# Kernel optimization log

Measured on AMD Instinct MI355X. Metric: run time of the kernel, lower is better.

Reference implementation:

```python
import jax, jax.numpy as jnp
import numpy as np

B, K, D = 8, 4000, 256
H, DQ, DV = 8, 32, 32
WIN, PAD = 200, 50
STEP = WIN - 2 * PAD  # 100
BETA = 0.25


def setup_inputs() -> dict:
    key = jax.random.key(0)
    ks = jax.random.split(key, 14)
    s = 0.02
    return {
        "query": jax.random.normal(ks[0], (B, K, D), jnp.float32),
        "key": jax.random.normal(ks[1], (B, K, D), jnp.float32),
        "value": jax.random.normal(ks[2], (B, K, D), jnp.float32),
        "Wq": jax.random.normal(ks[3], (D, H * DQ), jnp.float32) * s,
        "bq": jax.random.normal(ks[4], (H * DQ,), jnp.float32) * s,
        "Wk": jax.random.normal(ks[5], (D, H * DQ), jnp.float32) * s,
        "bk": jax.random.normal(ks[6], (H * DQ,), jnp.float32) * s,
        "Wv": jax.random.normal(ks[7], (D, H * DV), jnp.float32) * s,
        "bv": jax.random.normal(ks[8], (H * DV,), jnp.float32) * s,
        "Wo": jax.random.normal(ks[9], (H * DV, D), jnp.float32) * s,
        "bo": jax.random.normal(ks[10], (D,), jnp.float32) * s,
    }


def _windows(x, n_win):
    starts = jnp.arange(n_win) * STEP
    idx = starts[:, None] + jnp.arange(WIN)[None, :]
    return x[:, :, idx, :]


def reference(query, key, value, Wq, bq, Wk, bk, Wv, bv, Wo, bo):
    b, k_len, d = query.shape
    pad = lambda t: jnp.pad(t, ((0, 0), (PAD, PAD), (0, 0)), mode='edge')  # replicate pad
    qp, kp, vp = pad(query), pad(key), pad(value)
    kpad = k_len + 2 * PAD
    n_win = (kpad - WIN) // STEP + 1

    def proj(x, Wm, bias, dh):
        y = x @ Wm + bias                       # [B, Kp, H*dh]
        return y.reshape(b, kpad, H, dh).transpose(0, 2, 1, 3)  # [B, H, Kp, dh]

    q = _windows(proj(qp, Wq, bq, DQ), n_win)
    kk = _windows(proj(kp, Wk, bk, DQ), n_win)
    v = _windows(proj(vp, Wv, bv, DV), n_win)

    scores = jnp.einsum('bhnid,bhnjd->bhnij', q, kk) / jnp.sqrt(jnp.float32(WIN))
    dist = jnp.abs(jnp.arange(WIN)[:, None] - jnp.arange(WIN)[None, :]).astype(scores.dtype)
    cauchy = (1.0 / (1.0 + BETA * dist * dist)) * (1.0 - jnp.eye(WIN, dtype=scores.dtype))
    scores = scores * cauchy
    causal = jnp.triu(jnp.ones((WIN, WIN), dtype=bool), k=1)  # attention_size is not None -> causal masking
    scores = jnp.where(causal, -jnp.inf, scores)
    attn = jax.nn.softmax(scores, axis=-1)
    out = jnp.einsum('bhnij,bhnjd->bhnid', attn, v)
    out = out[:, :, :, PAD:WIN - PAD, :].reshape(b, H, k_len, DV)
    out = out.transpose(0, 2, 1, 3).reshape(b, k_len, H * DV)  # heads concatenated, head-major slices
    return out @ Wo + bo
```

## Files before the change

kernel.cpp:

```cpp
#include <hip/hip_runtime.h>


typedef __bf16 bf16_t;
typedef __bf16 bf16x4 __attribute__((ext_vector_type(4)));
typedef __bf16 bf16x8 __attribute__((ext_vector_type(8)));
typedef float  f32x4  __attribute__((ext_vector_type(4)));

#define MFMA16(a, b, c) __builtin_amdgcn_mfma_f32_16x16x32_bf16((a), (b), (c), 0, 0, 0)

typedef __attribute__((address_space(1))) const unsigned char gas_u8;
typedef __attribute__((address_space(3))) unsigned char las_u8;

static __device__ __forceinline__ void gload16(const void* g, void* l) {
  __builtin_amdgcn_global_load_lds((gas_u8*)g, (las_u8*)l, 16, 0, 0);
}

static __device__ __forceinline__ bf16x4 cvt4(float4 a) {
  bf16x4 r;
  r[0] = (bf16_t)a.x; r[1] = (bf16_t)a.y; r[2] = (bf16_t)a.z; r[3] = (bf16_t)a.w;
  return r;
}

static __device__ __forceinline__ unsigned short bbits(bf16_t v) {
  union { bf16_t b; unsigned short u; } c; c.b = v; return c.u;
}

#define APITCH 264
#define ABYTES (64 * APITCH * 2)

__global__ __launch_bounds__(256)
void prep_weights(const float* __restrict__ Wq, const float* __restrict__ Wk,
                  const float* __restrict__ Wv, const float* __restrict__ Wo,
                  bf16_t* __restrict__ wt) {
  const int mat  = blockIdx.x >> 6;
  const int tile = blockIdx.x & 63;
  const int kt = (tile >> 3) * 32, nt = (tile & 7) * 32;
  const float* W = (mat == 0) ? Wq : (mat == 1) ? Wk : (mat == 2) ? Wv : Wo;
  __shared__ float t[32][33];
  const int tx = threadIdx.x & 31, ty = threadIdx.x >> 5;
#pragma unroll
  for (int i = 0; i < 32; i += 8)
    t[ty + i][tx] = W[(size_t)(kt + ty + i) * 256 + nt + tx];
  __syncthreads();
  bf16_t* dst = wt + (size_t)mat * 65536;
#pragma unroll
  for (int i = 0; i < 32; i += 8)
    dst[(size_t)(nt + ty + i) * 256 + kt + tx] = (bf16_t)t[tx][ty + i];
}

__global__ __launch_bounds__(256)
void proj_gemm(const float* __restrict__ qx, const float* __restrict__ kx,
               const float* __restrict__ vx, const bf16_t* __restrict__ wt,
               const float* __restrict__ bq, const float* __restrict__ bk,
               const float* __restrict__ bv,
               bf16_t* __restrict__ qb, bf16_t* __restrict__ kb,
               bf16_t* __restrict__ vt, int M, float qscale) {
  const int mode = blockIdx.y;
  const float* X    = (mode == 0) ? qx : (mode == 1) ? kx : vx;
  const float* bias = (mode == 0) ? bq : (mode == 1) ? bk : bv;
  const bf16_t* W   = wt + (size_t)mode * 65536;

  __shared__ __align__(16) char lds[ABYTES + 2 * 16384];
  bf16_t* laA = (bf16_t*)lds;
  char*   ldsB = lds + ABYTES;

  const int tid  = threadIdx.x;
  const int lane = tid & 63;
  const int w    = tid >> 6;
  const int lo   = lane & 15, hi = lane >> 4;
  const int m0   = blockIdx.x * 64;

  {
    const int colq = (tid & 63) * 4;
    const int r0   = tid >> 6;
#pragma unroll
    for (int u = 0; u < 16; ++u) {
      const int r = r0 + u * 4;
      int ar = m0 + r; if (ar >= M) ar = M - 1;
      const float4 v = *(const float4*)(X + (size_t)ar * 256 + colq);
      *(bf16x4*)&laA[r * APITCH + colq] = cvt4(v);
    }
  }

  const bf16_t* bsrc[4];
  int boff[4];
#pragma unroll
  for (int j = 0; j < 4; ++j) {
    const int s = (w * 4 + j) * 64 + lane;
    bsrc[j] = W + (size_t)(s >> 2) * 256 + ((s & 3) << 3);
    boff[j] = (w * 4 + j) * 1024;
  }
  int bbase[4];
#pragma unroll
  for (int ni = 0; ni < 4; ++ni)
    bbase[ni] = (w * 64 + ni * 16 + lo) * 64 + hi * 16;

#pragma unroll
  for (int j = 0; j < 4; ++j) gload16(bsrc[j], ldsB + boff[j]);
  __syncthreads();

  f32x4 acc[4][4] = {};

  for (int t = 0; t < 8; ++t) {
    const int cur = (t & 1) * 16384;
    if (t < 7) {
      const int nxt = ((t + 1) & 1) * 16384;
#pragma unroll
      for (int j = 0; j < 4; ++j) gload16(bsrc[j] + (t + 1) * 32, ldsB + nxt + boff[j]);
      asm volatile("s_waitcnt vmcnt(4)" ::: "memory");
    } else {
      asm volatile("s_waitcnt vmcnt(0)" ::: "memory");
    }
    __builtin_amdgcn_sched_barrier(0);
    __builtin_amdgcn_s_barrier();

    bf16x8 af[4], bfv[4];
#pragma unroll
    for (int mi = 0; mi < 4; ++mi)
      af[mi] = *(const bf16x8*)&laA[(mi * 16 + lo) * APITCH + t * 32 + hi * 8];
#pragma unroll
    for (int ni = 0; ni < 4; ++ni)
      bfv[ni] = *(const bf16x8*)(ldsB + cur + bbase[ni]);
#pragma unroll
    for (int mi = 0; mi < 4; ++mi)
#pragma unroll
      for (int ni = 0; ni < 4; ++ni)
        acc[mi][ni] = MFMA16(af[mi], bfv[ni], acc[mi][ni]);
    __builtin_amdgcn_sched_barrier(0);
    __builtin_amdgcn_s_barrier();
  }

#pragma unroll
  for (int mi = 0; mi < 4; ++mi) {
    const int mb = m0 + mi * 16 + hi * 4;
    if (mb >= M) continue;
#pragma unroll
    for (int ni = 0; ni < 4; ++ni) {
      const int n = w * 64 + ni * 16 + lo;
      const float bia = bias[n];
      if (mode == 0) {
#pragma unroll
        for (int rr = 0; rr < 4; ++rr)
          qb[(size_t)(mb + rr) * 256 + n] = (bf16_t)((acc[mi][ni][rr] + bia) * qscale);
      } else if (mode == 1) {
        const int b = mb / 4000, t = mb - b * 4000;
#pragma unroll
        for (int rr = 0; rr < 4; ++rr) {
          const bf16_t v = (bf16_t)(acc[mi][ni][rr] + bia);
          kb[((size_t)b * 4064 + t + 50 + rr) * 256 + n] = v;
          if (t == 0 && rr == 0)
            for (int p = 0; p < 50; ++p)
              kb[((size_t)b * 4064 + p) * 256 + n] = v;
        }
      } else {
        const int b = mb / 4000, t = mb - b * 4000;
        const int h = n >> 5, dv = n & 31;
        const size_t vrow = ((size_t)((b * 8 + h) * 32 + dv)) * 4064;
        unsigned short e0 = bbits((bf16_t)(acc[mi][ni][0] + bia));
        unsigned short e1 = bbits((bf16_t)(acc[mi][ni][1] + bia));
        unsigned short e2 = bbits((bf16_t)(acc[mi][ni][2] + bia));
        unsigned short e3 = bbits((bf16_t)(acc[mi][ni][3] + bia));
        unsigned* O32 = (unsigned*)(vt + vrow + t + 50);
        O32[0] = (unsigned)e0 | ((unsigned)e1 << 16);
        O32[1] = (unsigned)e2 | ((unsigned)e3 << 16);
        if (t == 0) {
          const unsigned vv = (unsigned)e0 | ((unsigned)e0 << 16);
          unsigned* P = (unsigned*)(vt + vrow);
#pragma unroll
          for (int p = 0; p < 25; ++p) P[p] = vv;
        }
      }
    }
  }
}

__global__ __launch_bounds__(256)
void out_gemm(const bf16_t* __restrict__ ao, const bf16_t* __restrict__ wt,
              const float* __restrict__ bias, float* __restrict__ Out, int M) {
  __shared__ __align__(16) char lds[ABYTES + 2 * 16384];
  bf16_t* laA = (bf16_t*)lds;
  char*   ldsB = lds + ABYTES;

  const int tid  = threadIdx.x;
  const int lane = tid & 63;
  const int w    = tid >> 6;
  const int lo   = lane & 15, hi = lane >> 4;
  const int m0   = blockIdx.x * 64;

  {
    const int colb = (tid & 31) * 8;
    const int r0   = tid >> 5;
#pragma unroll
    for (int u = 0; u < 8; ++u) {
      const int r = r0 + u * 8;
      int ar = m0 + r; if (ar >= M) ar = M - 1;
      const bf16x8 v = *(const bf16x8*)(ao + (size_t)ar * 256 + colb);
      *(bf16x8*)&laA[r * APITCH + colb] = v;
    }
  }

  const bf16_t* bsrc[4];
  int boff[4];
#pragma unroll
  for (int j = 0; j < 4; ++j) {
    const int s = (w * 4 + j) * 64 + lane;
    bsrc[j] = wt + (size_t)(s >> 2) * 256 + ((s & 3) << 3);
    boff[j] = (w * 4 + j) * 1024;
  }
  int bbase[4];
#pragma unroll
  for (int ni = 0; ni < 4; ++ni)
    bbase[ni] = (w * 64 + ni * 16 + lo) * 64 + hi * 16;

#pragma unroll
  for (int j = 0; j < 4; ++j) gload16(bsrc[j], ldsB + boff[j]);
  __syncthreads();

  f32x4 acc[4][4] = {};

  for (int t = 0; t < 8; ++t) {
    const int cur = (t & 1) * 16384;
    if (t < 7) {
      const int nxt = ((t + 1) & 1) * 16384;
#pragma unroll
      for (int j = 0; j < 4; ++j) gload16(bsrc[j] + (t + 1) * 32, ldsB + nxt + boff[j]);
      asm volatile("s_waitcnt vmcnt(4)" ::: "memory");
    } else {
      asm volatile("s_waitcnt vmcnt(0)" ::: "memory");
    }
    __builtin_amdgcn_sched_barrier(0);
    __builtin_amdgcn_s_barrier();

    bf16x8 af[4], bfv[4];
#pragma unroll
    for (int mi = 0; mi < 4; ++mi)
      af[mi] = *(const bf16x8*)&laA[(mi * 16 + lo) * APITCH + t * 32 + hi * 8];
#pragma unroll
    for (int ni = 0; ni < 4; ++ni)
      bfv[ni] = *(const bf16x8*)(ldsB + cur + bbase[ni]);
#pragma unroll
    for (int mi = 0; mi < 4; ++mi)
#pragma unroll
      for (int ni = 0; ni < 4; ++ni)
        acc[mi][ni] = MFMA16(af[mi], bfv[ni], acc[mi][ni]);
    __builtin_amdgcn_sched_barrier(0);
    __builtin_amdgcn_s_barrier();
  }

#pragma unroll
  for (int mi = 0; mi < 4; ++mi) {
    const int mb = m0 + mi * 16 + hi * 4;
    if (mb >= M) continue;
#pragma unroll
    for (int ni = 0; ni < 4; ++ni) {
      const int n = w * 64 + ni * 16 + lo;
      const float bia = bias[n];
#pragma unroll
      for (int rr = 0; rr < 4; ++rr)
        Out[(size_t)(mb + rr) * 256 + n] = acc[mi][ni][rr] + bia;
    }
  }
}

__global__ __launch_bounds__(448)
void attn_win(const bf16_t* __restrict__ qb, const bf16_t* __restrict__ kb,
              const bf16_t* __restrict__ vt, bf16_t* __restrict__ ao) {
  const int blk = blockIdx.x;
  const int n = blk % 40;
  const int h = (blk / 40) & 7;
  const int b = blk / 320;
  const int wv = threadIdx.x >> 6;
  const int lane = threadIdx.x & 63;
  const int lo = lane & 15, hi = lane >> 4;

  __shared__ __align__(16) bf16_t E[7][16][40];

  const int i0 = 50 + 16 * wv;
  int jtmax = (65 + 16 * wv) >> 4;
  if (jtmax > 9) jtmax = 9;
  const int reach = jtmax * 16 + 16;

  int tq = n * 100 + 16 * wv + lo;
  if (tq > 3999) tq = 3999;
  const bf16x8 qf = *(const bf16x8*)&qb[((size_t)b * 4000 + tq) * 256 + h * 32 + hi * 8];

  const f32x4 zero = {0.f, 0.f, 0.f, 0.f};
  bf16x8 onesf;
#pragma unroll
  for (int u = 0; u < 8; ++u) onesf[u] = (bf16_t)1.0f;

  f32x4 o0 = zero, o1 = zero, sm = zero;
  const size_t vbase = ((size_t)((b * 8 + h) * 32)) * 4064 + n * 100;
  const size_t kbase = ((size_t)(b * 4064 + n * 100)) * 256 + h * 32 + hi * 8;
  const int dbase = i0 + hi * 4 - lo;

#pragma unroll
  for (int kt = 0; kt < 5; ++kt) if (kt * 32 < reach) {
#pragma unroll
    for (int half = 0; half < 2; ++half) {
      const int jt = kt * 2 + half;
      if (jt <= jtmax) {
        const bf16x8 kf = *(const bf16x8*)&kb[kbase + (size_t)(jt * 16 + lo) * 256];
        const f32x4 s = MFMA16(qf, kf, zero);
#pragma unroll
        for (int r = 0; r < 4; ++r) {
          const int d = dbase + r - jt * 16;
          const float df = (float)d;
          float c = __builtin_amdgcn_rcpf(__builtin_fmaf(0.25f * df, df, 1.f));
          c = (d == 0) ? 0.f : c;
          float e = __expf(s[r] * c);
          e = (d < 0) ? 0.f : e;
          E[wv][hi * 4 + r][half * 16 + lo] = (bf16_t)e;
        }
      } else {
#pragma unroll
        for (int r = 0; r < 4; ++r)
          E[wv][hi * 4 + r][half * 16 + lo] = (bf16_t)0.f;
      }
    }
    const bf16x8 pf = *(const bf16x8*)&E[wv][lo][hi * 8];
    const bf16x8 v0 = *(const bf16x8*)&vt[vbase + (size_t)lo * 4064 + kt * 32 + hi * 8];
    const bf16x8 v1 = *(const bf16x8*)&vt[vbase + (size_t)(16 + lo) * 4064 + kt * 32 + hi * 8];
    o0 = MFMA16(pf, v0, o0);
    o1 = MFMA16(pf, v1, o1);
    sm = MFMA16(pf, onesf, sm);
  }

#pragma unroll
  for (int r = 0; r < 4; ++r) {
    const int i = i0 + hi * 4 + r;
    if (i < 150) {
      const float ri = __builtin_amdgcn_rcpf(sm[r]);
      const int t = n * 100 + i - 50;
      bf16_t* op = &ao[((size_t)b * 4000 + t) * 256 + h * 32];
      op[lo]      = (bf16_t)(o0[r] * ri);
      op[16 + lo] = (bf16_t)(o1[r] * ri);
    }
  }
}

extern "C" void kernel_launch(void* const* d_in, const int* in_sizes, int n_in,
                              void* d_out, int out_size, void* d_ws, size_t ws_size,
                              hipStream_t stream) {
  (void)in_sizes; (void)n_in; (void)out_size;
  const float* query = (const float*)d_in[0];
  const float* key   = (const float*)d_in[1];
  const float* value = (const float*)d_in[2];
  const float* Wq = (const float*)d_in[3];
  const float* bq = (const float*)d_in[4];
  const float* Wk = (const float*)d_in[5];
  const float* bk = (const float*)d_in[6];
  const float* Wv = (const float*)d_in[7];
  const float* bv = (const float*)d_in[8];
  const float* Wo = (const float*)d_in[9];
  const float* bo = (const float*)d_in[10];

  int bc = 8;
  while (bc > 1 && 524288ull + (unsigned long long)bc * 8257536ull > (unsigned long long)ws_size)
    bc >>= 1;

  bf16_t* wt = (bf16_t*)d_ws;
  bf16_t* qb = wt + 4 * 65536;
  bf16_t* kb = qb + (size_t)bc * 4000 * 256;
  bf16_t* vt = kb + (size_t)bc * 4064 * 256;
  bf16_t* ao = vt + (size_t)bc * 8 * 32 * 4064;

  prep_weights<<<256, 256, 0, stream>>>(Wq, Wk, Wv, Wo, wt);

  const float qscale = 0.07071067811865475f;

  for (int b0 = 0; b0 < 8; b0 += bc) {
    const int M = bc * 4000;
    const int mblk = (M + 63) / 64;
    const float* qx = query + (size_t)b0 * 4000 * 256;
    const float* kx = key   + (size_t)b0 * 4000 * 256;
    const float* vx = value + (size_t)b0 * 4000 * 256;
    float* ox = (float*)d_out + (size_t)b0 * 4000 * 256;

    proj_gemm<<<dim3(mblk, 3), 256, 0, stream>>>(qx, kx, vx, wt, bq, bk, bv,
                                                 qb, kb, vt, M, qscale);
    attn_win<<<bc * 320, 448, 0, stream>>>(qb, kb, vt, ao);
    out_gemm<<<dim3(mblk), 256, 0, stream>>>(ao, wt + 3 * 65536, bo, ox, M);
  }
}
```

Before: 99.69 us.

## Stage V projection transpose through LDS and write 16-byte vectors to Vt

The V projection epilogue now writes its tile transposed into shared memory and then issues 16-byte vectorized stores to the transposed V buffer. Before, each lane made scattered 4-byte stores. Vt rows are offset by 6 elements so the data region starts 16-byte aligned, and the attention kernel's V base is shifted to match. Projection blocks are re-tiled per batch (63 tiles of 64 rows each), so no tile straddles a batch boundary. This adds an extra barrier and reuses the LDS A buffer, which grows to 256x72 for the transpose.

```diff
diff --git a/kernel.cpp b/kernel.cpp
--- a/kernel.cpp
+++ b/kernel.cpp
@@ -26,7 +26,8 @@
 }
 
 #define APITCH 264
-#define ABYTES (64 * APITCH * 2)
+#define TPITCH 72
+#define LDSA_BYTES (256 * TPITCH * 2)
 
 __global__ __launch_bounds__(256)
 void prep_weights(const float* __restrict__ Wq, const float* __restrict__ Wk,
@@ -54,21 +55,23 @@
                const float* __restrict__ bq, const float* __restrict__ bk,
                const float* __restrict__ bv,
                bf16_t* __restrict__ qb, bf16_t* __restrict__ kb,
-               bf16_t* __restrict__ vt, int M, float qscale) {
+               bf16_t* __restrict__ vt, float qscale) {
   const int mode = blockIdx.y;
   const float* X    = (mode == 0) ? qx : (mode == 1) ? kx : vx;
   const float* bias = (mode == 0) ? bq : (mode == 1) ? bk : bv;
   const bf16_t* W   = wt + (size_t)mode * 65536;
 
-  __shared__ __align__(16) char lds[ABYTES + 2 * 16384];
+  __shared__ __align__(16) char lds[LDSA_BYTES + 2 * 16384];
   bf16_t* laA = (bf16_t*)lds;
-  char*   ldsB = lds + ABYTES;
+  char*   ldsB = lds + LDSA_BYTES;
 
   const int tid  = threadIdx.x;
   const int lane = tid & 63;
   const int w    = tid >> 6;
   const int lo   = lane & 15, hi = lane >> 4;
-  const int m0   = blockIdx.x * 64;
+  const int bL   = blockIdx.x / 63;
+  const int t0   = (blockIdx.x % 63) * 64;
+  const int tmax = 4000 - t0;
 
   {
     const int colq = (tid & 63) * 4;
@@ -76,8 +79,8 @@
 #pragma unroll
     for (int u = 0; u < 16; ++u) {
       const int r = r0 + u * 4;
-      int ar = m0 + r; if (ar >= M) ar = M - 1;
-      const float4 v = *(const float4*)(X + (size_t)ar * 256 + colq);
+      int t = t0 + r; if (t > 3999) t = 3999;
+      const float4 v = *(const float4*)(X + ((size_t)bL * 4000 + t) * 256 + colq);
       *(bf16x4*)&laA[r * APITCH + colq] = cvt4(v);
     }
   }
@@ -130,46 +133,64 @@
     __builtin_amdgcn_s_barrier();
   }
 
-#pragma unroll
-  for (int mi = 0; mi < 4; ++mi) {
-    const int mb = m0 + mi * 16 + hi * 4;
-    if (mb >= M) continue;
-#pragma unroll
-    for (int ni = 0; ni < 4; ++ni) {
-      const int n = w * 64 + ni * 16 + lo;
-      const float bia = bias[n];
-      if (mode == 0) {
-#pragma unroll
-        for (int rr = 0; rr < 4; ++rr)
-          qb[(size_t)(mb + rr) * 256 + n] = (bf16_t)((acc[mi][ni][rr] + bia) * qscale);
-      } else if (mode == 1) {
-        const int b = mb / 4000, t = mb - b * 4000;
+  if (mode != 2) {
+#pragma unroll
+    for (int mi = 0; mi < 4; ++mi) {
+#pragma unroll
+      for (int ni = 0; ni < 4; ++ni) {
+        const int n = w * 64 + ni * 16 + lo;
+        const float bia = bias[n];
 #pragma unroll
         for (int rr = 0; rr < 4; ++rr) {
-          const bf16_t v = (bf16_t)(acc[mi][ni][rr] + bia);
-          kb[((size_t)b * 4064 + t + 50 + rr) * 256 + n] = v;
-          if (t == 0 && rr == 0)
-            for (int p = 0; p < 50; ++p)
-              kb[((size_t)b * 4064 + p) * 256 + n] = v;
-        }
-      } else {
-        const int b = mb / 4000, t = mb - b * 4000;
-        const int h = n >> 5, dv = n & 31;
-        const size_t vrow = ((size_t)((b * 8 + h) * 32 + dv)) * 4064;
-        unsigned short e0 = bbits((bf16_t)(acc[mi][ni][0] + bia));
-        unsigned short e1 = bbits((bf16_t)(acc[mi][ni][1] + bia));
-        unsigned short e2 = bbits((bf16_t)(acc[mi][ni][2] + bia));
-        unsigned short e3 = bbits((bf16_t)(acc[mi][ni][3] + bia));
-        unsigned* O32 = (unsigned*)(vt + vrow + t + 50);
-        O32[0] = (unsigned)e0 | ((unsigned)e1 << 16);
-        O32[1] = (unsigned)e2 | ((unsigned)e3 << 16);
-        if (t == 0) {
-          const unsigned vv = (unsigned)e0 | ((unsigned)e0 << 16);
-          unsigned* P = (unsigned*)(vt + vrow);
-#pragma unroll
-          for (int p = 0; p < 25; ++p) P[p] = vv;
+          const int tl = mi * 16 + hi * 4 + rr;
+          if (tl >= tmax) continue;
+          const int t = t0 + tl;
+          if (mode == 0) {
+            qb[((size_t)bL * 4000 + t) * 256 + n] =
+                (bf16_t)((acc[mi][ni][rr] + bia) * qscale);
+          } else {
+            const bf16_t v = (bf16_t)(acc[mi][ni][rr] + bia);
+            kb[((size_t)bL * 4064 + t + 50) * 256 + n] = v;
+            if (t == 0)
+              for (int p = 0; p < 50; ++p)
+                kb[((size_t)bL * 4064 + p) * 256 + n] = v;
+          }
         }
       }
+    }
+  } else {
+    bf16_t* T = (bf16_t*)lds;
+#pragma unroll
+    for (int mi = 0; mi < 4; ++mi) {
+      const int tl = mi * 16 + hi * 4;
+#pragma unroll
+      for (int ni = 0; ni < 4; ++ni) {
+        const int n = w * 64 + ni * 16 + lo;
+        const float bia = bias[n];
+        unsigned* dst = (unsigned*)&T[n * TPITCH + tl];
+        dst[0] = (unsigned)bbits((bf16_t)(acc[mi][ni][0] + bia)) |
+                 ((unsigned)bbits((bf16_t)(acc[mi][ni][1] + bia)) << 16);
+        dst[1] = (unsigned)bbits((bf16_t)(acc[mi][ni][2] + bia)) |
+                 ((unsigned)bbits((bf16_t)(acc[mi][ni][3] + bia)) << 16);
+      }
+    }
+    __syncthreads();
+    const int c = lane & 7;
+    const bf16_t* Trow0 = T + (w * 64 + (lane >> 3)) * TPITCH;
+    bf16_t* vrow0 = vt + ((size_t)bL * 256 + (w * 64 + (lane >> 3))) * 4064 + 56 + t0;
+#pragma unroll
+    for (int g = 0; g < 8; ++g) {
+      if (c * 8 + 8 <= tmax) {
+        const bf16x8 v = *(const bf16x8*)(Trow0 + g * 8 * TPITCH + c * 8);
+        *(bf16x8*)(vrow0 + (size_t)g * 8 * 4064 + c * 8) = v;
+      }
+    }
+    if (t0 == 0) {
+      const unsigned short e = bbits(T[tid * TPITCH]);
+      const unsigned vv = (unsigned)e | ((unsigned)e << 16);
+      unsigned* P = (unsigned*)(vt + ((size_t)bL * 256 + tid) * 4064 + 6);
+#pragma unroll
+      for (int p = 0; p < 25; ++p) P[p] = vv;
     }
   }
 }
@@ -177,9 +198,9 @@
 __global__ __launch_bounds__(256)
 void out_gemm(const bf16_t* __restrict__ ao, const bf16_t* __restrict__ wt,
               const float* __restrict__ bias, float* __restrict__ Out, int M) {
-  __shared__ __align__(16) char lds[ABYTES + 2 * 16384];
+  __shared__ __align__(16) char lds[64 * APITCH * 2 + 2 * 16384];
   bf16_t* laA = (bf16_t*)lds;
-  char*   ldsB = lds + ABYTES;
+  char*   ldsB = lds + 64 * APITCH * 2;
 
   const int tid  = threadIdx.x;
   const int lane = tid & 63;
@@ -290,7 +311,7 @@
   for (int u = 0; u < 8; ++u) onesf[u] = (bf16_t)1.0f;
 
   f32x4 o0 = zero, o1 = zero, sm = zero;
-  const size_t vbase = ((size_t)((b * 8 + h) * 32)) * 4064 + n * 100;
+  const size_t vbase = ((size_t)((b * 8 + h) * 32)) * 4064 + n * 100 + 6;
   const size_t kbase = ((size_t)(b * 4064 + n * 100)) * 256 + h * 32 + hi * 8;
   const int dbase = i0 + hi * 4 - lo;
 
@@ -363,7 +384,7 @@
   bf16_t* qb = wt + 4 * 65536;
   bf16_t* kb = qb + (size_t)bc * 4000 * 256;
   bf16_t* vt = kb + (size_t)bc * 4064 * 256;
-  bf16_t* ao = vt + (size_t)bc * 8 * 32 * 4064;
+  bf16_t* ao = vt + (size_t)bc * 256 * 4064;
 
   prep_weights<<<256, 256, 0, stream>>>(Wq, Wk, Wv, Wo, wt);
 
@@ -371,15 +392,14 @@
 
   for (int b0 = 0; b0 < 8; b0 += bc) {
     const int M = bc * 4000;
-    const int mblk = (M + 63) / 64;
     const float* qx = query + (size_t)b0 * 4000 * 256;
     const float* kx = key   + (size_t)b0 * 4000 * 256;
     const float* vx = value + (size_t)b0 * 4000 * 256;
     float* ox = (float*)d_out + (size_t)b0 * 4000 * 256;
 
-    proj_gemm<<<dim3(mblk, 3), 256, 0, stream>>>(qx, kx, vx, wt, bq, bk, bv,
-                                                 qb, kb, vt, M, qscale);
+    proj_gemm<<<dim3(63 * bc, 3), 256, 0, stream>>>(qx, kx, vx, wt, bq, bk, bv,
+                                                    qb, kb, vt, qscale);
     attn_win<<<bc * 320, 448, 0, stream>>>(qb, kb, vt, ao);
-    out_gemm<<<dim3(mblk), 256, 0, stream>>>(ao, wt + 3 * 65536, bo, ox, M);
-  }
-}
+    out_gemm<<<dim3((M + 63) / 64), 256, 0, stream>>>(ao, wt + 3 * 65536, bo, ox, M);
+  }
+}
```

Result: no change. 99.84 us (+0.2%).
